# Performance work log

Hardware: AMD Instinct MI355X
Metric: run time of the kernel (lower is better)

Reference implementation:

```python
import jax, jax.numpy as jnp
import numpy as np

EMBED_DIM = 1024
NUM_HEADS = 16
HEAD_DIM = EMBED_DIM // NUM_HEADS
BATCH = 2
SEQ = 2048


def setup_inputs() -> dict:
    key = jax.random.key(0)
    ks = jax.random.split(key, 9)
    scale = 1.0 / np.sqrt(EMBED_DIM)
    return {
        "inputs": jax.random.normal(ks[0], (BATCH, SEQ, EMBED_DIM), jnp.float32),
        "Wq": jax.random.normal(ks[1], (EMBED_DIM, EMBED_DIM), jnp.float32) * scale,
        "bq": jnp.zeros((EMBED_DIM,), jnp.float32),
        "Wk": jax.random.normal(ks[2], (EMBED_DIM, EMBED_DIM), jnp.float32) * scale,
        "bk": jnp.zeros((EMBED_DIM,), jnp.float32),
        "Wv": jax.random.normal(ks[3], (EMBED_DIM, EMBED_DIM), jnp.float32) * scale,
        "bv": jnp.zeros((EMBED_DIM,), jnp.float32),
        "Wo": jax.random.normal(ks[4], (EMBED_DIM, EMBED_DIM), jnp.float32) * scale,
        "bo": jnp.zeros((EMBED_DIM,), jnp.float32),
    }


def reference(inputs, Wq, bq, Wk, bk, Wv, bv, Wo, bo):
    B, S, D = inputs.shape
    H, Dh = NUM_HEADS, HEAD_DIM

    def split_heads(x):  # [B,S,D] -> [B,H,S,Dh]
        return x.reshape(B, S, H, Dh).transpose(0, 2, 1, 3)

    Q = split_heads(inputs @ Wq + bq)
    K = split_heads(inputs @ Wk + bk)
    V = split_heads(inputs @ Wv + bv)

    # naive full-score attention, faithful to the original
    scores = jnp.einsum("bhqd,bhkd->bhqk", Q, K) / jnp.sqrt(jnp.float32(Dh))
    weights = jax.nn.softmax(scores, axis=-1)
    out = jnp.einsum("bhqk,bhkd->bhqd", weights, V)

    concat = out.transpose(0, 2, 1, 3).reshape(B, S, D)
    return concat @ Wo + bo
```

## Files before the change

### kernel.cpp

```cpp
#include <hip/hip_runtime.h>

#define EMBED 1024
#define NHEAD 16
#define HDIM  64
#define BATCH 2
#define SEQ   2048
#define MTOK  (BATCH * SEQ)
#define QSCALE 0.1803368801f

typedef __bf16 bf16x8 __attribute__((ext_vector_type(8)));
typedef float  f32x4  __attribute__((ext_vector_type(4)));

__device__ __forceinline__ unsigned short f2bf(float f) {
  return (unsigned short)((__float_as_uint(f) + 0x8000u) >> 16);
}
__device__ __forceinline__ unsigned int pkbf(float a, float b) {
  unsigned int ua = __float_as_uint(a) + 0x8000u;
  unsigned int ub = __float_as_uint(b) + 0x8000u;
  return __builtin_amdgcn_perm(ub, ua, 0x07060302u);
}

__device__ __forceinline__ void gload_lds16(const unsigned short* g, unsigned short* l) {
  __builtin_amdgcn_global_load_lds((__attribute__((address_space(1))) void*)g,
                                   (__attribute__((address_space(3))) void*)l, 16, 0, 0);
}

__global__ __launch_bounds__(256)
void prep_k(const float* __restrict__ X, unsigned short* __restrict__ Xbf,
            const float* __restrict__ w0, const float* __restrict__ w1,
            const float* __restrict__ w2, const float* __restrict__ w3,
            unsigned short* __restrict__ t0, unsigned short* __restrict__ t1,
            unsigned short* __restrict__ t2, unsigned short* __restrict__ t3) {
  const int id = blockIdx.x;
  if (id < 4096) {
    int i = id * 256 + threadIdx.x;
    float4 f = reinterpret_cast<const float4*>(X)[i];
    reinterpret_cast<uint2*>(Xbf)[i] = make_uint2(pkbf(f.x, f.y), pkbf(f.z, f.w));
    return;
  }
  const int t = id - 4096;
  const float* s; unsigned short* d;
  switch (t >> 8) {
    case 0: s = w0; d = t0; break;
    case 1: s = w1; d = t1; break;
    case 2: s = w2; d = t2; break;
    default: s = w3; d = t3; break;
  }
  const int tt = t & 255;
  const int k0 = (tt >> 4) * 64, n0 = (tt & 15) * 64;
  __shared__ unsigned short T[64][65];
  for (int i = threadIdx.x; i < 4096; i += 256) {
    int r = i >> 6, c = i & 63;
    T[c][r] = f2bf(s[(size_t)(k0 + r) * EMBED + n0 + c]);
  }
  __syncthreads();
  for (int i = threadIdx.x; i < 4096; i += 256) {
    int r = i >> 6, c = i & 63;
    d[(size_t)(n0 + r) * EMBED + k0 + c] = T[r][c];
  }
}

template<int MODE, int BM>
__global__ void gemm_k(const unsigned short* __restrict__ A,
                       const unsigned short* __restrict__ Bt,
                       const float* __restrict__ b0, const float* __restrict__ b1,
                       const float* __restrict__ b2,
                       unsigned short* __restrict__ oQ, unsigned short* __restrict__ oK,
                       unsigned short* __restrict__ oV, float* __restrict__ oF) {
  constexpr int MI = BM / 32;
  __shared__ unsigned short As[BM][64];
  __shared__ unsigned short Bs[128][64];
  const int tid = threadIdx.x, lane = tid & 63, wave = tid >> 6;
  const int lr = lane & 15, quad = lane >> 4;
  const int wm = (wave >> 1) * (BM / 2), wn = (wave & 1) * 64;
  const int row0 = blockIdx.x * BM, col0 = blockIdx.y * 128;
  const int srow = lane >> 3, sc = lane & 7;
  const int sw0 = (quad ^ (lr & 7)) * 8;
  const int sw1 = ((quad ^ 4) ^ (lr & 7)) * 8;

  const f32x4 fz = {0.f, 0.f, 0.f, 0.f};
  f32x4 acc[MI][4];
#pragma unroll
  for (int i = 0; i < MI; ++i)
#pragma unroll
    for (int j = 0; j < 4; ++j) acc[i][j] = fz;

  for (int k0 = 0; k0 < EMBED; k0 += 64) {
#pragma unroll
    for (int g = 0; g < BM / 32; ++g) {
      int rbase = wave * (BM / 4) + g * 8;
      int row = rbase + srow;
      gload_lds16(&A[(size_t)(row0 + row) * EMBED + k0 + ((sc ^ (row & 7)) * 8)],
                  &As[rbase][0]);
    }
#pragma unroll
    for (int g = 0; g < 4; ++g) {
      int rbase = wave * 32 + g * 8;
      int row = rbase + srow;
      gload_lds16(&Bt[(size_t)(col0 + row) * EMBED + k0 + ((sc ^ (row & 7)) * 8)],
                  &Bs[rbase][0]);
    }
    __syncthreads();
#pragma unroll
    for (int kk = 0; kk < 64; kk += 32) {
      const int so = (kk == 0) ? sw0 : sw1;
      bf16x8 af[MI], bv[4];
#pragma unroll
      for (int i = 0; i < MI; ++i)
        af[i] = *reinterpret_cast<const bf16x8*>(&As[wm + i * 16 + lr][so]);
#pragma unroll
      for (int j = 0; j < 4; ++j)
        bv[j] = *reinterpret_cast<const bf16x8*>(&Bs[wn + j * 16 + lr][so]);
#pragma unroll
      for (int i = 0; i < MI; ++i)
#pragma unroll
        for (int j = 0; j < 4; ++j)
          acc[i][j] = __builtin_amdgcn_mfma_f32_16x16x32_bf16(af[i], bv[j],
                                                              acc[i][j], 0, 0, 0);
    }
    __syncthreads();
  }

#pragma unroll
  for (int i = 0; i < MI; ++i) {
#pragma unroll
    for (int j = 0; j < 4; ++j) {
      const int col = col0 + wn + j * 16 + lr;
      if (MODE == 1) {
        const float bb = b0[col];
#pragma unroll
        for (int r = 0; r < 4; ++r) {
          const int row = row0 + wm + i * 16 + quad * 4 + r;
          oF[((size_t)row << 10) + col] = acc[i][j][r] + bb;
        }
      } else {
        const int which = col >> 10, cn = col & 1023;
        const float bb = (which == 0 ? b0 : which == 1 ? b1 : b2)[cn];
        const float sscale = (which == 0) ? QSCALE : 1.0f;
        const int h = cn >> 6, dd = cn & 63;
#pragma unroll
        for (int r = 0; r < 4; ++r) {
          const int row = row0 + wm + i * 16 + quad * 4 + r;
          const int b = row >> 11, ss = row & (SEQ - 1);
          const float v = (acc[i][j][r] + bb) * sscale;
          if (which == 0) {
            oQ[((((size_t)b * NHEAD + h) * SEQ + ss) << 6) + dd] = f2bf(v);
          } else if (which == 1) {
            oK[((((size_t)b * NHEAD + h) * SEQ + ss) << 6) + dd] = f2bf(v);
          } else {
            oV[(((size_t)b * NHEAD + h) * HDIM + dd) * SEQ + ss] = f2bf(v);
          }
        }
      }
    }
  }
}

__global__ __launch_bounds__(256, 6)
void attn_k(const unsigned short* __restrict__ Qb,
            const unsigned short* __restrict__ Kb,
            const unsigned short* __restrict__ Vt,
            unsigned short* __restrict__ Ctx) {
  __shared__ unsigned short QPs[64][64];
  __shared__ unsigned short Ks[64][64];
  __shared__ unsigned short Vs[64][64];
  const int tid = threadIdx.x, lane = tid & 63, wave = tid >> 6;
  const int lr = lane & 15, quad = lane >> 4;
  const int bh = blockIdx.x, qt = blockIdx.y;
  const size_t base = (size_t)bh * SEQ * HDIM;
  const int srow = lane >> 3, sc = lane & 7;
  const int sw0 = (quad ^ (lr & 7)) * 8;
  const int sw1 = ((quad ^ 4) ^ (lr & 7)) * 8;

#pragma unroll
  for (int g = 0; g < 2; ++g) {
    int rbase = wave * 16 + g * 8;
    int row = rbase + srow;
    gload_lds16(&Qb[base + (size_t)(qt * 64 + row) * HDIM + ((sc ^ (row & 7)) * 8)],
                &QPs[rbase][0]);
    gload_lds16(&Kb[base + (size_t)row * HDIM + ((sc ^ (row & 7)) * 8)], &Ks[rbase][0]);
    gload_lds16(&Vt[base + (size_t)row * SEQ + ((sc ^ (row & 7)) * 8)], &Vs[rbase][0]);
  }
  __syncthreads();

  const bf16x8 qf0 = *reinterpret_cast<const bf16x8*>(&QPs[wave * 16 + lr][sw0]);
  const bf16x8 qf1 = *reinterpret_cast<const bf16x8*>(&QPs[wave * 16 + lr][sw1]);
  __threadfence_block();

  float l_part = 0.f;
  const f32x4 fz = {0.f, 0.f, 0.f, 0.f};
  f32x4 oacc[4] = {fz, fz, fz, fz};

  for (int kt = 0;;) {
    f32x4 sc4[4];
#pragma unroll
    for (int nt = 0; nt < 4; ++nt) {
      bf16x8 kf0 = *reinterpret_cast<const bf16x8*>(&Ks[nt * 16 + lr][sw0]);
      bf16x8 kf1 = *reinterpret_cast<const bf16x8*>(&Ks[nt * 16 + lr][sw1]);
      f32x4 a = __builtin_amdgcn_mfma_f32_16x16x32_bf16(kf0, qf0, fz, 0, 0, 0);
      sc4[nt] = __builtin_amdgcn_mfma_f32_16x16x32_bf16(kf1, qf1, a, 0, 0, 0);
    }

#pragma unroll
    for (int nt = 0; nt < 4; ++nt) {
      float p0 = __builtin_amdgcn_exp2f(sc4[nt][0]);
      float p1 = __builtin_amdgcn_exp2f(sc4[nt][1]);
      float p2 = __builtin_amdgcn_exp2f(sc4[nt][2]);
      float p3 = __builtin_amdgcn_exp2f(sc4[nt][3]);
      l_part += (p0 + p1) + (p2 + p3);
      const int pc = (nt * 2 + (quad >> 1)) ^ (lr & 7);
      *reinterpret_cast<uint2*>(&QPs[wave * 16 + lr][pc * 8 + (quad & 1) * 4]) =
          make_uint2(pkbf(p0, p1), pkbf(p2, p3));
    }

    __threadfence_block();

    const bf16x8 pa0 = *reinterpret_cast<const bf16x8*>(&QPs[wave * 16 + lr][sw0]);
    const bf16x8 pa1 = *reinterpret_cast<const bf16x8*>(&QPs[wave * 16 + lr][sw1]);
#pragma unroll
    for (int d = 0; d < 4; ++d) {
      bf16x8 vb0 = *reinterpret_cast<const bf16x8*>(&Vs[d * 16 + lr][sw0]);
      bf16x8 vb1 = *reinterpret_cast<const bf16x8*>(&Vs[d * 16 + lr][sw1]);
      oacc[d] = __builtin_amdgcn_mfma_f32_16x16x32_bf16(pa0, vb0, oacc[d], 0, 0, 0);
      oacc[d] = __builtin_amdgcn_mfma_f32_16x16x32_bf16(pa1, vb1, oacc[d], 0, 0, 0);
    }

    if (++kt == SEQ / 64) break;
    __syncthreads();
#pragma unroll
    for (int g = 0; g < 2; ++g) {
      int rbase = wave * 16 + g * 8;
      int row = rbase + srow;
      gload_lds16(&Kb[base + (size_t)(kt * 64 + row) * HDIM + ((sc ^ (row & 7)) * 8)],
                  &Ks[rbase][0]);
      gload_lds16(&Vt[base + (size_t)row * SEQ + kt * 64 + ((sc ^ (row & 7)) * 8)],
                  &Vs[rbase][0]);
    }
    __syncthreads();
  }

  l_part += __shfl_xor(l_part, 16);
  l_part += __shfl_xor(l_part, 32);

  const int b = bh >> 4, h = bh & 15;
  float linv[4];
#pragma unroll
  for (int r = 0; r < 4; ++r) linv[r] = 1.0f / __shfl(l_part, quad * 4 + r);
#pragma unroll
  for (int d = 0; d < 4; ++d)
#pragma unroll
    for (int r = 0; r < 4; ++r) {
      const int q = qt * 64 + wave * 16 + quad * 4 + r;
      Ctx[(((size_t)b * SEQ + q) << 10) + h * 64 + d * 16 + lr] =
          f2bf(oacc[d][r] * linv[r]);
    }
}

extern "C" void kernel_launch(void* const* d_in, const int* in_sizes, int n_in,
                              void* d_out, int out_size, void* d_ws, size_t ws_size,
                              hipStream_t stream) {
  const float* X  = (const float*)d_in[0];
  const float* Wq = (const float*)d_in[1];
  const float* bq = (const float*)d_in[2];
  const float* Wk = (const float*)d_in[3];
  const float* bk = (const float*)d_in[4];
  const float* Wv = (const float*)d_in[5];
  const float* bv = (const float*)d_in[6];
  const float* Wo = (const float*)d_in[7];
  const float* bo = (const float*)d_in[8];

  unsigned short* ws = (unsigned short*)d_ws;
  const size_t M1 = (size_t)1024 * 1024;
  unsigned short* Xbf = ws;
  unsigned short* WqT = ws + 4 * M1;
  unsigned short* WkT = ws + 5 * M1;
  unsigned short* WvT = ws + 6 * M1;
  unsigned short* WoT = ws + 7 * M1;
  unsigned short* Qb  = ws + 8 * M1;
  unsigned short* Kb  = ws + 12 * M1;
  unsigned short* Vt  = ws + 16 * M1;
  unsigned short* Ctx = ws + 20 * M1;

  prep_k<<<5120, 256, 0, stream>>>(X, Xbf, Wq, Wk, Wv, Wo, WqT, WkT, WvT, WoT);

  gemm_k<0, 128><<<dim3(MTOK / 128, 3072 / 128), 256, 0, stream>>>(
      Xbf, WqT, bq, bk, bv, Qb, Kb, Vt, nullptr);

  attn_k<<<dim3(BATCH * NHEAD, SEQ / 64), 256, 0, stream>>>(Qb, Kb, Vt, Ctx);

  gemm_k<1, 64><<<dim3(MTOK / 64, EMBED / 128), 256, 0, stream>>>(
      Ctx, WoT, bo, nullptr, nullptr, nullptr, nullptr, nullptr, (float*)d_out);
}
```

Before: 193.8 us.

## Double-buffer K/V tiles in attention kernel to overlap loads with MFMA

Splits the K and V shared-memory tiles into two buffers and issues the next tile's global-to-LDS loads at the top of each iteration, so they can proceed while the current tile's QK and PV MFMAs run. This removes one barrier per iteration and hides load latency behind compute. In exchange it raises LDS use from 24KB to 40KB per block and lowers the occupancy hint from 6 to 4 blocks per CU. Correctness depends on the remaining barrier at the loop end covering both the async LDS writes and the reuse of the buffer.

```diff
diff --git a/kernel.cpp b/kernel.cpp
--- a/kernel.cpp
+++ b/kernel.cpp
@@ -156,14 +156,14 @@
   }
 }
 
-__global__ __launch_bounds__(256, 6)
+__global__ __launch_bounds__(256, 4)
 void attn_k(const unsigned short* __restrict__ Qb,
             const unsigned short* __restrict__ Kb,
             const unsigned short* __restrict__ Vt,
             unsigned short* __restrict__ Ctx) {
   __shared__ unsigned short QPs[64][64];
-  __shared__ unsigned short Ks[64][64];
-  __shared__ unsigned short Vs[64][64];
+  __shared__ unsigned short Ks[2][64][64];
+  __shared__ unsigned short Vs[2][64][64];
   const int tid = threadIdx.x, lane = tid & 63, wave = tid >> 6;
   const int lr = lane & 15, quad = lane >> 4;
   const int bh = blockIdx.x, qt = blockIdx.y;
@@ -178,8 +178,10 @@
     int row = rbase + srow;
     gload_lds16(&Qb[base + (size_t)(qt * 64 + row) * HDIM + ((sc ^ (row & 7)) * 8)],
                 &QPs[rbase][0]);
-    gload_lds16(&Kb[base + (size_t)row * HDIM + ((sc ^ (row & 7)) * 8)], &Ks[rbase][0]);
-    gload_lds16(&Vt[base + (size_t)row * SEQ + ((sc ^ (row & 7)) * 8)], &Vs[rbase][0]);
+    gload_lds16(&Kb[base + (size_t)row * HDIM + ((sc ^ (row & 7)) * 8)],
+                &Ks[0][rbase][0]);
+    gload_lds16(&Vt[base + (size_t)row * SEQ + ((sc ^ (row & 7)) * 8)],
+                &Vs[0][rbase][0]);
   }
   __syncthreads();
 
@@ -191,12 +193,27 @@
   const f32x4 fz = {0.f, 0.f, 0.f, 0.f};
   f32x4 oacc[4] = {fz, fz, fz, fz};
 
+  constexpr int NT = SEQ / 64;
   for (int kt = 0;;) {
+    const int buf = kt & 1;
+
+    if (kt + 1 < NT) {
+#pragma unroll
+      for (int g = 0; g < 2; ++g) {
+        int rbase = wave * 16 + g * 8;
+        int row = rbase + srow;
+        gload_lds16(&Kb[base + (size_t)((kt + 1) * 64 + row) * HDIM + ((sc ^ (row & 7)) * 8)],
+                    &Ks[buf ^ 1][rbase][0]);
+        gload_lds16(&Vt[base + (size_t)row * SEQ + (kt + 1) * 64 + ((sc ^ (row & 7)) * 8)],
+                    &Vs[buf ^ 1][rbase][0]);
+      }
+    }
+
     f32x4 sc4[4];
 #pragma unroll
     for (int nt = 0; nt < 4; ++nt) {
-      bf16x8 kf0 = *reinterpret_cast<const bf16x8*>(&Ks[nt * 16 + lr][sw0]);
-      bf16x8 kf1 = *reinterpret_cast<const bf16x8*>(&Ks[nt * 16 + lr][sw1]);
+      bf16x8 kf0 = *reinterpret_cast<const bf16x8*>(&Ks[buf][nt * 16 + lr][sw0]);
+      bf16x8 kf1 = *reinterpret_cast<const bf16x8*>(&Ks[buf][nt * 16 + lr][sw1]);
       f32x4 a = __builtin_amdgcn_mfma_f32_16x16x32_bf16(kf0, qf0, fz, 0, 0, 0);
       sc4[nt] = __builtin_amdgcn_mfma_f32_16x16x32_bf16(kf1, qf1, a, 0, 0, 0);
     }
@@ -219,23 +236,13 @@
     const bf16x8 pa1 = *reinterpret_cast<const bf16x8*>(&QPs[wave * 16 + lr][sw1]);
 #pragma unroll
     for (int d = 0; d < 4; ++d) {
-      bf16x8 vb0 = *reinterpret_cast<const bf16x8*>(&Vs[d * 16 + lr][sw0]);
-      bf16x8 vb1 = *reinterpret_cast<const bf16x8*>(&Vs[d * 16 + lr][sw1]);
+      bf16x8 vb0 = *reinterpret_cast<const bf16x8*>(&Vs[buf][d * 16 + lr][sw0]);
+      bf16x8 vb1 = *reinterpret_cast<const bf16x8*>(&Vs[buf][d * 16 + lr][sw1]);
       oacc[d] = __builtin_amdgcn_mfma_f32_16x16x32_bf16(pa0, vb0, oacc[d], 0, 0, 0);
       oacc[d] = __builtin_amdgcn_mfma_f32_16x16x32_bf16(pa1, vb1, oacc[d], 0, 0, 0);
     }
 
-    if (++kt == SEQ / 64) break;
-    __syncthreads();
-#pragma unroll
-    for (int g = 0; g < 2; ++g) {
-      int rbase = wave * 16 + g * 8;
-      int row = rbase + srow;
-      gload_lds16(&Kb[base + (size_t)(kt * 64 + row) * HDIM + ((sc ^ (row & 7)) * 8)],
-                  &Ks[rbase][0]);
-      gload_lds16(&Vt[base + (size_t)row * SEQ + kt * 64 + ((sc ^ (row & 7)) * 8)],
-                  &Vs[rbase][0]);
-    }
+    if (++kt == NT) break;
     __syncthreads();
   }
 
```

After: 191.0 us. No clear change (-1.4%).

## Warp-specialize GEMM with producer waves double-buffering LDS tiles

Applied to the files above, without the earlier changes.

The GEMM kernel now launches 512 threads, where four producer waves issue global-to-LDS loads for the next K tile into a second buffer while four consumer waves run MFMA on the current buffer. This is meant to overlap global memory latency with matrix compute, which the single-buffered loop serialized. In exchange LDS use doubles, block size grows, and there is still one barrier per K step. Producer waves are idle during the epilogue.

```diff
diff --git a/kernel.cpp b/kernel.cpp
--- a/kernel.cpp
+++ b/kernel.cpp
@@ -61,16 +61,19 @@
 }
 
 template<int MODE, int BM>
-__global__ void gemm_k(const unsigned short* __restrict__ A,
-                       const unsigned short* __restrict__ Bt,
-                       const float* __restrict__ b0, const float* __restrict__ b1,
-                       const float* __restrict__ b2,
-                       unsigned short* __restrict__ oQ, unsigned short* __restrict__ oK,
-                       unsigned short* __restrict__ oV, float* __restrict__ oF) {
+__global__ __launch_bounds__(512, 4)
+void gemm_k(const unsigned short* __restrict__ A,
+            const unsigned short* __restrict__ Bt,
+            const float* __restrict__ b0, const float* __restrict__ b1,
+            const float* __restrict__ b2,
+            unsigned short* __restrict__ oQ, unsigned short* __restrict__ oK,
+            unsigned short* __restrict__ oV, float* __restrict__ oF) {
   constexpr int MI = BM / 32;
-  __shared__ unsigned short As[BM][64];
-  __shared__ unsigned short Bs[128][64];
+  __shared__ unsigned short As[2][BM][64];
+  __shared__ unsigned short Bs[2][128][64];
   const int tid = threadIdx.x, lane = tid & 63, wave = tid >> 6;
+  const bool producer = wave >= 4;
+  const int pw = wave & 3;
   const int lr = lane & 15, quad = lane >> 4;
   const int wm = (wave >> 1) * (BM / 2), wn = (wave & 1) * 64;
   const int row0 = blockIdx.x * BM, col0 = blockIdx.y * 128;
@@ -78,6 +81,23 @@
   const int sw0 = (quad ^ (lr & 7)) * 8;
   const int sw1 = ((quad ^ 4) ^ (lr & 7)) * 8;
 
+  auto stage = [&](int k0, int b) {
+#pragma unroll
+    for (int g = 0; g < BM / 32; ++g) {
+      int rbase = pw * (BM / 4) + g * 8;
+      int row = rbase + srow;
+      gload_lds16(&A[(size_t)(row0 + row) * EMBED + k0 + ((sc ^ (row & 7)) * 8)],
+                  &As[b][rbase][0]);
+    }
+#pragma unroll
+    for (int g = 0; g < 4; ++g) {
+      int rbase = pw * 32 + g * 8;
+      int row = rbase + srow;
+      gload_lds16(&Bt[(size_t)(col0 + row) * EMBED + k0 + ((sc ^ (row & 7)) * 8)],
+                  &Bs[b][rbase][0]);
+    }
+  };
+
   const f32x4 fz = {0.f, 0.f, 0.f, 0.f};
   f32x4 acc[MI][4];
 #pragma unroll
@@ -85,42 +105,36 @@
 #pragma unroll
     for (int j = 0; j < 4; ++j) acc[i][j] = fz;
 
+  if (producer) stage(0, 0);
+  __syncthreads();
+
   for (int k0 = 0; k0 < EMBED; k0 += 64) {
-#pragma unroll
-    for (int g = 0; g < BM / 32; ++g) {
-      int rbase = wave * (BM / 4) + g * 8;
-      int row = rbase + srow;
-      gload_lds16(&A[(size_t)(row0 + row) * EMBED + k0 + ((sc ^ (row & 7)) * 8)],
-                  &As[rbase][0]);
-    }
-#pragma unroll
-    for (int g = 0; g < 4; ++g) {
-      int rbase = wave * 32 + g * 8;
-      int row = rbase + srow;
-      gload_lds16(&Bt[(size_t)(col0 + row) * EMBED + k0 + ((sc ^ (row & 7)) * 8)],
-                  &Bs[rbase][0]);
+    const int b = (k0 >> 6) & 1;
+    if (producer) {
+      if (k0 + 64 < EMBED) stage(k0 + 64, b ^ 1);
+    } else {
+#pragma unroll
+      for (int kk = 0; kk < 64; kk += 32) {
+        const int so = (kk == 0) ? sw0 : sw1;
+        bf16x8 af[MI], bv[4];
+#pragma unroll
+        for (int i = 0; i < MI; ++i)
+          af[i] = *reinterpret_cast<const bf16x8*>(&As[b][wm + i * 16 + lr][so]);
+#pragma unroll
+        for (int j = 0; j < 4; ++j)
+          bv[j] = *reinterpret_cast<const bf16x8*>(&Bs[b][wn + j * 16 + lr][so]);
+#pragma unroll
+        for (int i = 0; i < MI; ++i)
+#pragma unroll
+          for (int j = 0; j < 4; ++j)
+            acc[i][j] = __builtin_amdgcn_mfma_f32_16x16x32_bf16(af[i], bv[j],
+                                                                acc[i][j], 0, 0, 0);
+      }
     }
     __syncthreads();
-#pragma unroll
-    for (int kk = 0; kk < 64; kk += 32) {
-      const int so = (kk == 0) ? sw0 : sw1;
-      bf16x8 af[MI], bv[4];
-#pragma unroll
-      for (int i = 0; i < MI; ++i)
-        af[i] = *reinterpret_cast<const bf16x8*>(&As[wm + i * 16 + lr][so]);
-#pragma unroll
-      for (int j = 0; j < 4; ++j)
-        bv[j] = *reinterpret_cast<const bf16x8*>(&Bs[wn + j * 16 + lr][so]);
-#pragma unroll
-      for (int i = 0; i < MI; ++i)
-#pragma unroll
-        for (int j = 0; j < 4; ++j)
-          acc[i][j] = __builtin_amdgcn_mfma_f32_16x16x32_bf16(af[i], bv[j],
-                                                              acc[i][j], 0, 0, 0);
-    }
-    __syncthreads();
-  }
-
+  }
+
+  if (producer) return;
 #pragma unroll
   for (int i = 0; i < MI; ++i) {
 #pragma unroll
@@ -141,14 +155,14 @@
 #pragma unroll
         for (int r = 0; r < 4; ++r) {
           const int row = row0 + wm + i * 16 + quad * 4 + r;
-          const int b = row >> 11, ss = row & (SEQ - 1);
+          const int b2i = row >> 11, ss = row & (SEQ - 1);
           const float v = (acc[i][j][r] + bb) * sscale;
           if (which == 0) {
-            oQ[((((size_t)b * NHEAD + h) * SEQ + ss) << 6) + dd] = f2bf(v);
+            oQ[((((size_t)b2i * NHEAD + h) * SEQ + ss) << 6) + dd] = f2bf(v);
           } else if (which == 1) {
-            oK[((((size_t)b * NHEAD + h) * SEQ + ss) << 6) + dd] = f2bf(v);
+            oK[((((size_t)b2i * NHEAD + h) * SEQ + ss) << 6) + dd] = f2bf(v);
           } else {
-            oV[(((size_t)b * NHEAD + h) * HDIM + dd) * SEQ + ss] = f2bf(v);
+            oV[(((size_t)b2i * NHEAD + h) * HDIM + dd) * SEQ + ss] = f2bf(v);
           }
         }
       }
@@ -283,11 +297,11 @@
 
   prep_k<<<5120, 256, 0, stream>>>(X, Xbf, Wq, Wk, Wv, Wo, WqT, WkT, WvT, WoT);
 
-  gemm_k<0, 128><<<dim3(MTOK / 128, 3072 / 128), 256, 0, stream>>>(
+  gemm_k<0, 128><<<dim3(MTOK / 128, 3072 / 128), 512, 0, stream>>>(
       Xbf, WqT, bq, bk, bv, Qb, Kb, Vt, nullptr);
 
   attn_k<<<dim3(BATCH * NHEAD, SEQ / 64), 256, 0, stream>>>(Qb, Kb, Vt, Ctx);
 
-  gemm_k<1, 64><<<dim3(MTOK / 64, EMBED / 128), 256, 0, stream>>>(
+  gemm_k<1, 64><<<dim3(MTOK / 64, EMBED / 128), 512, 0, stream>>>(
       Ctx, WoT, bo, nullptr, nullptr, nullptr, nullptr, nullptr, (float*)d_out);
 }
```

Result: slower. 205.8 us (+6.2%).

## Process two query sub-tiles per wave in attention to reuse K/V tiles

Applied to the files above, without the earlier changes.

The attention kernel now handles 128 queries per block, 32 per wave as two 16-row groups, so each K and V tile loaded into LDS serves twice as many queries. This halves the K/V global traffic and the per-tile LDS fragment reads of K and V relative to the compute. In exchange it raises register and LDS use, lowers the occupancy target from 6 to 4, and halves the grid to 512 blocks, which cuts parallelism on a large GPU.

```diff
diff --git a/kernel.cpp b/kernel.cpp
--- a/kernel.cpp
+++ b/kernel.cpp
@@ -156,12 +156,12 @@
   }
 }
 
-__global__ __launch_bounds__(256, 6)
+__global__ __launch_bounds__(256, 4)
 void attn_k(const unsigned short* __restrict__ Qb,
             const unsigned short* __restrict__ Kb,
             const unsigned short* __restrict__ Vt,
             unsigned short* __restrict__ Ctx) {
-  __shared__ unsigned short QPs[64][64];
+  __shared__ unsigned short QPs[128][64];
   __shared__ unsigned short Ks[64][64];
   __shared__ unsigned short Vs[64][64];
   const int tid = threadIdx.x, lane = tid & 63, wave = tid >> 6;
@@ -173,56 +173,84 @@
   const int sw1 = ((quad ^ 4) ^ (lr & 7)) * 8;
 
 #pragma unroll
+  for (int g = 0; g < 4; ++g) {
+    int rbase = wave * 32 + g * 8;
+    int row = rbase + srow;
+    gload_lds16(&Qb[base + (size_t)(qt * 128 + row) * HDIM + ((sc ^ (row & 7)) * 8)],
+                &QPs[rbase][0]);
+  }
+#pragma unroll
   for (int g = 0; g < 2; ++g) {
     int rbase = wave * 16 + g * 8;
     int row = rbase + srow;
-    gload_lds16(&Qb[base + (size_t)(qt * 64 + row) * HDIM + ((sc ^ (row & 7)) * 8)],
-                &QPs[rbase][0]);
     gload_lds16(&Kb[base + (size_t)row * HDIM + ((sc ^ (row & 7)) * 8)], &Ks[rbase][0]);
     gload_lds16(&Vt[base + (size_t)row * SEQ + ((sc ^ (row & 7)) * 8)], &Vs[rbase][0]);
   }
   __syncthreads();
 
-  const bf16x8 qf0 = *reinterpret_cast<const bf16x8*>(&QPs[wave * 16 + lr][sw0]);
-  const bf16x8 qf1 = *reinterpret_cast<const bf16x8*>(&QPs[wave * 16 + lr][sw1]);
+  bf16x8 qf[2][2];
+#pragma unroll
+  for (int qg = 0; qg < 2; ++qg) {
+    qf[qg][0] = *reinterpret_cast<const bf16x8*>(&QPs[wave * 32 + qg * 16 + lr][sw0]);
+    qf[qg][1] = *reinterpret_cast<const bf16x8*>(&QPs[wave * 32 + qg * 16 + lr][sw1]);
+  }
   __threadfence_block();
 
-  float l_part = 0.f;
+  float l_part[2] = {0.f, 0.f};
   const f32x4 fz = {0.f, 0.f, 0.f, 0.f};
-  f32x4 oacc[4] = {fz, fz, fz, fz};
+  f32x4 oacc[2][4];
+#pragma unroll
+  for (int qg = 0; qg < 2; ++qg)
+#pragma unroll
+    for (int d = 0; d < 4; ++d) oacc[qg][d] = fz;
 
   for (int kt = 0;;) {
-    f32x4 sc4[4];
+    f32x4 sc4[2][4];
 #pragma unroll
     for (int nt = 0; nt < 4; ++nt) {
       bf16x8 kf0 = *reinterpret_cast<const bf16x8*>(&Ks[nt * 16 + lr][sw0]);
       bf16x8 kf1 = *reinterpret_cast<const bf16x8*>(&Ks[nt * 16 + lr][sw1]);
-      f32x4 a = __builtin_amdgcn_mfma_f32_16x16x32_bf16(kf0, qf0, fz, 0, 0, 0);
-      sc4[nt] = __builtin_amdgcn_mfma_f32_16x16x32_bf16(kf1, qf1, a, 0, 0, 0);
-    }
-
-#pragma unroll
-    for (int nt = 0; nt < 4; ++nt) {
-      float p0 = __builtin_amdgcn_exp2f(sc4[nt][0]);
-      float p1 = __builtin_amdgcn_exp2f(sc4[nt][1]);
-      float p2 = __builtin_amdgcn_exp2f(sc4[nt][2]);
-      float p3 = __builtin_amdgcn_exp2f(sc4[nt][3]);
-      l_part += (p0 + p1) + (p2 + p3);
-      const int pc = (nt * 2 + (quad >> 1)) ^ (lr & 7);
-      *reinterpret_cast<uint2*>(&QPs[wave * 16 + lr][pc * 8 + (quad & 1) * 4]) =
-          make_uint2(pkbf(p0, p1), pkbf(p2, p3));
-    }
+#pragma unroll
+      for (int qg = 0; qg < 2; ++qg) {
+        f32x4 a = __builtin_amdgcn_mfma_f32_16x16x32_bf16(kf0, qf[qg][0], fz, 0, 0, 0);
+        sc4[qg][nt] = __builtin_amdgcn_mfma_f32_16x16x32_bf16(kf1, qf[qg][1], a, 0, 0, 0);
+      }
+    }
+
+#pragma unroll
+    for (int qg = 0; qg < 2; ++qg)
+#pragma unroll
+      for (int nt = 0; nt < 4; ++nt) {
+        float p0 = __builtin_amdgcn_exp2f(sc4[qg][nt][0]);
+        float p1 = __builtin_amdgcn_exp2f(sc4[qg][nt][1]);
+        float p2 = __builtin_amdgcn_exp2f(sc4[qg][nt][2]);
+        float p3 = __builtin_amdgcn_exp2f(sc4[qg][nt][3]);
+        l_part[qg] += (p0 + p1) + (p2 + p3);
+        const int pc = (nt * 2 + (quad >> 1)) ^ (lr & 7);
+        *reinterpret_cast<uint2*>(
+            &QPs[wave * 32 + qg * 16 + lr][pc * 8 + (quad & 1) * 4]) =
+            make_uint2(pkbf(p0, p1), pkbf(p2, p3));
+      }
 
     __threadfence_block();
 
-    const bf16x8 pa0 = *reinterpret_cast<const bf16x8*>(&QPs[wave * 16 + lr][sw0]);
-    const bf16x8 pa1 = *reinterpret_cast<const bf16x8*>(&QPs[wave * 16 + lr][sw1]);
+    bf16x8 pa[2][2];
+#pragma unroll
+    for (int qg = 0; qg < 2; ++qg) {
+      pa[qg][0] = *reinterpret_cast<const bf16x8*>(&QPs[wave * 32 + qg * 16 + lr][sw0]);
+      pa[qg][1] = *reinterpret_cast<const bf16x8*>(&QPs[wave * 32 + qg * 16 + lr][sw1]);
+    }
 #pragma unroll
     for (int d = 0; d < 4; ++d) {
       bf16x8 vb0 = *reinterpret_cast<const bf16x8*>(&Vs[d * 16 + lr][sw0]);
       bf16x8 vb1 = *reinterpret_cast<const bf16x8*>(&Vs[d * 16 + lr][sw1]);
-      oacc[d] = __builtin_amdgcn_mfma_f32_16x16x32_bf16(pa0, vb0, oacc[d], 0, 0, 0);
-      oacc[d] = __builtin_amdgcn_mfma_f32_16x16x32_bf16(pa1, vb1, oacc[d], 0, 0, 0);
+#pragma unroll
+      for (int qg = 0; qg < 2; ++qg) {
+        oacc[qg][d] = __builtin_amdgcn_mfma_f32_16x16x32_bf16(pa[qg][0], vb0,
+                                                              oacc[qg][d], 0, 0, 0);
+        oacc[qg][d] = __builtin_amdgcn_mfma_f32_16x16x32_bf16(pa[qg][1], vb1,
+                                                              oacc[qg][d], 0, 0, 0);
+      }
     }
 
     if (++kt == SEQ / 64) break;
@@ -239,21 +267,24 @@
     __syncthreads();
   }
 
-  l_part += __shfl_xor(l_part, 16);
-  l_part += __shfl_xor(l_part, 32);
-
   const int b = bh >> 4, h = bh & 15;
-  float linv[4];
-#pragma unroll
-  for (int r = 0; r < 4; ++r) linv[r] = 1.0f / __shfl(l_part, quad * 4 + r);
-#pragma unroll
-  for (int d = 0; d < 4; ++d)
-#pragma unroll
-    for (int r = 0; r < 4; ++r) {
-      const int q = qt * 64 + wave * 16 + quad * 4 + r;
-      Ctx[(((size_t)b * SEQ + q) << 10) + h * 64 + d * 16 + lr] =
-          f2bf(oacc[d][r] * linv[r]);
-    }
+#pragma unroll
+  for (int qg = 0; qg < 2; ++qg) {
+    float lp = l_part[qg];
+    lp += __shfl_xor(lp, 16);
+    lp += __shfl_xor(lp, 32);
+    float linv[4];
+#pragma unroll
+    for (int r = 0; r < 4; ++r) linv[r] = 1.0f / __shfl(lp, quad * 4 + r);
+#pragma unroll
+    for (int d = 0; d < 4; ++d)
+#pragma unroll
+      for (int r = 0; r < 4; ++r) {
+        const int q = qt * 128 + wave * 32 + qg * 16 + quad * 4 + r;
+        Ctx[(((size_t)b * SEQ + q) << 10) + h * 64 + d * 16 + lr] =
+            f2bf(oacc[qg][d][r] * linv[r]);
+      }
+  }
 }
 
 extern "C" void kernel_launch(void* const* d_in, const int* in_sizes, int n_in,
@@ -286,7 +317,7 @@
   gemm_k<0, 128><<<dim3(MTOK / 128, 3072 / 128), 256, 0, stream>>>(
       Xbf, WqT, bq, bk, bv, Qb, Kb, Vt, nullptr);
 
-  attn_k<<<dim3(BATCH * NHEAD, SEQ / 64), 256, 0, stream>>>(Qb, Kb, Vt, Ctx);
+  attn_k<<<dim3(BATCH * NHEAD, SEQ / 128), 256, 0, stream>>>(Qb, Kb, Vt, Ctx);
 
   gemm_k<1, 64><<<dim3(MTOK / 64, EMBED / 128), 256, 0, stream>>>(
       Ctx, WoT, bo, nullptr, nullptr, nullptr, nullptr, nullptr, (float*)d_out);
```

Measured after the change: 194.7 us. Within noise of the previous version (+0.5%).
